# Kernel tuning notes

Measured on AMD Instinct MI355X. Metric: run time of the kernel, lower is better.

## Reference

```python
import jax, jax.numpy as jnp
import numpy as np

S, B, E, H = 2048, 2, 1024, 16
D = E // H  # head_dim


def setup_inputs() -> dict:
    key = jax.random.key(0)
    ks = jax.random.split(key, 12)
    scale = 1.0 / np.sqrt(E)
    inp = {
        "query": jax.random.normal(ks[0], (S, B, E), jnp.float32),
        "key_": jax.random.normal(ks[1], (S, B, E), jnp.float32),
        "value": jax.random.normal(ks[2], (S, B, E), jnp.float32),
        "Wq": jax.random.normal(ks[3], (E, E), jnp.float32) * scale,
        "bq": jax.random.normal(ks[4], (E,), jnp.float32) * scale,
        "Wk": jax.random.normal(ks[5], (E, E), jnp.float32) * scale,
        "bk": jax.random.normal(ks[6], (E,), jnp.float32) * scale,
        "Wv": jax.random.normal(ks[7], (E, E), jnp.float32) * scale,
        "bv": jax.random.normal(ks[8], (E,), jnp.float32) * scale,
        "Wo": jax.random.normal(ks[9], (E, E), jnp.float32) * scale,
        "bo": jax.random.normal(ks[10], (E,), jnp.float32) * scale,
        "bias_matrix": jax.random.normal(ks[11], (S, S), jnp.float32) * 0.1,
    }
    return inp


def _proj(x, W, b):
    # x: [S,B,E] -> linear -> [B,H,S,D]
    y = jnp.einsum('sbe,fe->sbf', x, W) + b  # torch Linear: x @ W.T + b
    return y.transpose(1, 0, 2).reshape(B, S, H, D).transpose(0, 2, 1, 3)


def reference(query, key_, value, Wq, bq, Wk, bk, Wv, bv, Wo, bo, bias_matrix):
    scaling = D ** -0.5
    Q = _proj(query, Wq, bq)   # [B,H,S,D]
    K = _proj(key_, Wk, bk)
    V = _proj(value, Wv, bv)
    scores = jnp.einsum('bhqd,bhkd->bhqk', Q, K) * scaling
    scores = scores + bias_matrix[None, None, :, :]
    attn = jax.nn.softmax(scores, axis=-1)  # dropout=0.0
    context = jnp.einsum('bhqk,bhkd->bhqd', attn, V)
    context = context.transpose(0, 2, 1, 3).reshape(B, S, E)
    out = jnp.einsum('bse,fe->bsf', context, Wo) + bo
    return out.transpose(1, 0, 2), attn  # ([S,B,E], [B,H,S,S])
```

## Files before the change

kernel.cpp:

```cpp
#include <hip/hip_runtime.h>

#define S_LEN 2048
#define B_SZ  2
#define E_SZ  1024
#define H_SZ  16
#define D_SZ  64

typedef __attribute__((ext_vector_type(8))) _Float16 f16x8;
typedef __attribute__((ext_vector_type(4))) _Float16 f16x4;
typedef __attribute__((ext_vector_type(4))) float    f32x4;

#define MFMA16(A,B,C) __builtin_amdgcn_mfma_f32_16x16x32_f16(A,B,C,0,0,0)

__device__ __forceinline__ void splitf(float x, _Float16& h, _Float16& l)
{
    _Float16 hh = (_Float16)x;
    h = hh;
    l = (_Float16)((x - (float)hh) * 2048.0f);
}

__device__ __forceinline__ void split_store4(float4 v, _Float16* ph, _Float16* pl)
{
    _Float16 h0,h1,h2,h3,l0,l1,l2,l3;
    splitf(v.x,h0,l0); splitf(v.y,h1,l1); splitf(v.z,h2,l2); splitf(v.w,h3,l3);
    *(f16x4*)ph = (f16x4){h0,h1,h2,h3};
    *(f16x4*)pl = (f16x4){l0,l1,l2,l3};
}

template<int VT>
__global__ __launch_bounds__(256, 2) void proj_qkv_mfma(
    const float* __restrict__ X,
    const float* __restrict__ W,
    const float* __restrict__ bias,
    _Float16* __restrict__ Oh, _Float16* __restrict__ Ol)
{
    __shared__ __align__(16) _Float16 sAh[64][32];
    __shared__ __align__(16) _Float16 sAl[64][32];
    __shared__ __align__(16) _Float16 sBh[128][32];
    __shared__ __align__(16) _Float16 sBl[128][32];

    const int t  = threadIdx.x;
    const int w  = t >> 6;
    const int l  = t & 63;
    const int lr = l & 15;
    const int lg = l >> 4;
    const int kb = lg * 8;
    const int m0 = blockIdx.y * 64;
    const int n0 = blockIdx.x * 128;

    const int srow = t >> 3;
    const int sc4  = (t & 7) * 4;

    f32x4 acc_h[4][2] = {};
    f32x4 acc_x[4][2] = {};

    for (int k0 = 0; k0 < E_SZ; k0 += 32) {
        #pragma unroll
        for (int i = 0; i < 2; ++i) {
            int row = srow + 32 * i;
            float4 v = *(const float4*)&X[(size_t)(m0 + row) * E_SZ + k0 + sc4];
            split_store4(v, &sAh[row][sc4], &sAl[row][sc4]);
        }
        #pragma unroll
        for (int i = 0; i < 4; ++i) {
            int row = srow + 32 * i;
            float4 v = *(const float4*)&W[(size_t)(n0 + row) * E_SZ + k0 + sc4];
            split_store4(v, &sBh[row][sc4], &sBl[row][sc4]);
        }
        __syncthreads();

        f16x8 fah[4], fal[4], fbh[2], fbl[2];
        #pragma unroll
        for (int mt = 0; mt < 4; ++mt) {
            fah[mt] = *(const f16x8*)&sAh[mt*16 + lr][kb];
            fal[mt] = *(const f16x8*)&sAl[mt*16 + lr][kb];
        }
        #pragma unroll
        for (int nt = 0; nt < 2; ++nt) {
            fbh[nt] = *(const f16x8*)&sBh[w*32 + nt*16 + lr][kb];
            fbl[nt] = *(const f16x8*)&sBl[w*32 + nt*16 + lr][kb];
        }
        #pragma unroll
        for (int mt = 0; mt < 4; ++mt)
            #pragma unroll
            for (int nt = 0; nt < 2; ++nt) {
                acc_h[mt][nt] = MFMA16(fah[mt], fbh[nt], acc_h[mt][nt]);
                acc_x[mt][nt] = MFMA16(fah[mt], fbl[nt], acc_x[mt][nt]);
                acc_x[mt][nt] = MFMA16(fal[mt], fbh[nt], acc_x[mt][nt]);
            }
        __syncthreads();
    }

    #pragma unroll
    for (int nt = 0; nt < 2; ++nt) {
        int c = n0 + w*32 + nt*16 + lr;
        float bv = bias[c];
        int hh = c >> 6, d = c & 63;
        #pragma unroll
        for (int mt = 0; mt < 4; ++mt)
            #pragma unroll
            for (int j = 0; j < 4; ++j) {
                int r = m0 + mt*16 + lg*4 + j;
                int s = r >> 1, b = r & 1;
                float v = acc_h[mt][nt][j] + acc_x[mt][nt][j] * (1.0f/2048.0f) + bv;
                _Float16 vh, vl; splitf(v, vh, vl);
                size_t idx = VT ? ((size_t)((b*H_SZ + hh)*D_SZ + d)) * S_LEN + s
                                : ((size_t)((b*H_SZ + hh)*S_LEN + s)) * D_SZ + d;
                Oh[idx] = vh; Ol[idx] = vl;
            }
    }
}

__global__ __launch_bounds__(256, 2) void proj_out_mfma(
    const float* __restrict__ X,
    const float* __restrict__ W,
    const float* __restrict__ bias,
    float* __restrict__ out)
{
    __shared__ __align__(16) _Float16 sAh[64][32];
    __shared__ __align__(16) _Float16 sAl[64][32];
    __shared__ __align__(16) _Float16 sBh[128][32];
    __shared__ __align__(16) _Float16 sBl[128][32];

    const int t  = threadIdx.x;
    const int w  = t >> 6;
    const int l  = t & 63;
    const int lr = l & 15;
    const int lg = l >> 4;
    const int kb = lg * 8;
    const int m0 = blockIdx.y * 64;
    const int n0 = blockIdx.x * 128;

    const int srow = t >> 3;
    const int sc4  = (t & 7) * 4;

    f32x4 acc_h[4][2] = {};
    f32x4 acc_x[4][2] = {};

    for (int k0 = 0; k0 < E_SZ; k0 += 32) {
        #pragma unroll
        for (int i = 0; i < 2; ++i) {
            int row = srow + 32 * i;
            float4 v = *(const float4*)&X[(size_t)(m0 + row) * E_SZ + k0 + sc4];
            split_store4(v, &sAh[row][sc4], &sAl[row][sc4]);
        }
        #pragma unroll
        for (int i = 0; i < 4; ++i) {
            int row = srow + 32 * i;
            float4 v = *(const float4*)&W[(size_t)(n0 + row) * E_SZ + k0 + sc4];
            split_store4(v, &sBh[row][sc4], &sBl[row][sc4]);
        }
        __syncthreads();

        f16x8 fah[4], fal[4], fbh[2], fbl[2];
        #pragma unroll
        for (int mt = 0; mt < 4; ++mt) {
            fah[mt] = *(const f16x8*)&sAh[mt*16 + lr][kb];
            fal[mt] = *(const f16x8*)&sAl[mt*16 + lr][kb];
        }
        #pragma unroll
        for (int nt = 0; nt < 2; ++nt) {
            fbh[nt] = *(const f16x8*)&sBh[w*32 + nt*16 + lr][kb];
            fbl[nt] = *(const f16x8*)&sBl[w*32 + nt*16 + lr][kb];
        }
        #pragma unroll
        for (int mt = 0; mt < 4; ++mt)
            #pragma unroll
            for (int nt = 0; nt < 2; ++nt) {
                acc_h[mt][nt] = MFMA16(fah[mt], fbh[nt], acc_h[mt][nt]);
                acc_x[mt][nt] = MFMA16(fah[mt], fbl[nt], acc_x[mt][nt]);
                acc_x[mt][nt] = MFMA16(fal[mt], fbh[nt], acc_x[mt][nt]);
            }
        __syncthreads();
    }

    #pragma unroll
    for (int nt = 0; nt < 2; ++nt) {
        int c = n0 + w*32 + nt*16 + lr;
        float bv = bias[c];
        #pragma unroll
        for (int mt = 0; mt < 4; ++mt)
            #pragma unroll
            for (int j = 0; j < 4; ++j) {
                int r = m0 + mt*16 + lg*4 + j;
                int b = r >> 11, s = r & 2047;
                float v = acc_h[mt][nt][j] + acc_x[mt][nt][j] * (1.0f/2048.0f) + bv;
                out[((size_t)s * B_SZ + b) * E_SZ + c] = v;
            }
    }
}

__global__ __launch_bounds__(256, 2) void scores_mfma(
    const _Float16* __restrict__ Qh, const _Float16* __restrict__ Ql,
    const _Float16* __restrict__ Kh, const _Float16* __restrict__ Kl,
    const float* __restrict__ biasM, float* __restrict__ attn)
{
    __shared__ __align__(16) _Float16 sQh[128][32];
    __shared__ __align__(16) _Float16 sQl[128][32];
    __shared__ __align__(16) _Float16 sKh[128][32];
    __shared__ __align__(16) _Float16 sKl[128][32];

    const int t  = threadIdx.x;
    const int w  = t >> 6;
    const int l  = t & 63;
    const int lr = l & 15;
    const int lg = l >> 4;
    const int kb = lg * 8;
    const int wm = w >> 1, wn = w & 1;
    const int kc0 = blockIdx.x * 128;
    const int q0  = blockIdx.y * 128;
    const int bh  = blockIdx.z;

    const _Float16* gQh = Qh + (size_t)(bh * S_LEN + q0)  * D_SZ;
    const _Float16* gQl = Ql + (size_t)(bh * S_LEN + q0)  * D_SZ;
    const _Float16* gKh = Kh + (size_t)(bh * S_LEN + kc0) * D_SZ;
    const _Float16* gKl = Kl + (size_t)(bh * S_LEN + kc0) * D_SZ;

    const int srow = t >> 2;
    const int sch  = (t & 3) * 8;

    f32x4 acc_h[4][4] = {};
    f32x4 acc_x[4][4] = {};

    #pragma unroll
    for (int k0 = 0; k0 < D_SZ; k0 += 32) {
        #pragma unroll
        for (int i = 0; i < 2; ++i) {
            int row = srow + 64 * i;
            *(f16x8*)&sQh[row][sch] = *(const f16x8*)&gQh[(size_t)row * D_SZ + k0 + sch];
            *(f16x8*)&sQl[row][sch] = *(const f16x8*)&gQl[(size_t)row * D_SZ + k0 + sch];
            *(f16x8*)&sKh[row][sch] = *(const f16x8*)&gKh[(size_t)row * D_SZ + k0 + sch];
            *(f16x8*)&sKl[row][sch] = *(const f16x8*)&gKl[(size_t)row * D_SZ + k0 + sch];
        }
        __syncthreads();

        f16x8 fah[4], fal[4], fbh[4], fbl[4];
        #pragma unroll
        for (int i = 0; i < 4; ++i) {
            fah[i] = *(const f16x8*)&sQh[wm*64 + i*16 + lr][kb];
            fal[i] = *(const f16x8*)&sQl[wm*64 + i*16 + lr][kb];
            fbh[i] = *(const f16x8*)&sKh[wn*64 + i*16 + lr][kb];
            fbl[i] = *(const f16x8*)&sKl[wn*64 + i*16 + lr][kb];
        }
        #pragma unroll
        for (int mt = 0; mt < 4; ++mt)
            #pragma unroll
            for (int nt = 0; nt < 4; ++nt) {
                acc_h[mt][nt] = MFMA16(fah[mt], fbh[nt], acc_h[mt][nt]);
                acc_x[mt][nt] = MFMA16(fah[mt], fbl[nt], acc_x[mt][nt]);
                acc_x[mt][nt] = MFMA16(fal[mt], fbh[nt], acc_x[mt][nt]);
            }
        __syncthreads();
    }

    const float scale = 0.125f;
    #pragma unroll
    for (int mt = 0; mt < 4; ++mt)
        #pragma unroll
        for (int j = 0; j < 4; ++j) {
            int q = q0 + wm*64 + mt*16 + lg*4 + j;
            const float* bR = biasM + (size_t)q * S_LEN;
            float* oR = attn + ((size_t)bh * S_LEN + q) * S_LEN;
            #pragma unroll
            for (int nt = 0; nt < 4; ++nt) {
                int kc = kc0 + wn*64 + nt*16 + lr;
                float v = acc_h[mt][nt][j] + acc_x[mt][nt][j] * (1.0f/2048.0f);
                oR[kc] = v * scale + bR[kc];
            }
        }
}

__global__ __launch_bounds__(256) void softmax_kernel(float* __restrict__ attn)
{
    const size_t row = blockIdx.x;
    float* p = attn + row * S_LEN;
    const int t = threadIdx.x;

    float4 v0 = *(const float4*)&p[t * 4];
    float4 v1 = *(const float4*)&p[1024 + t * 4];
    float v[8] = {v0.x, v0.y, v0.z, v0.w, v1.x, v1.y, v1.z, v1.w};

    float m = v[0];
    #pragma unroll
    for (int i = 1; i < 8; ++i) m = fmaxf(m, v[i]);
    #pragma unroll
    for (int off = 32; off; off >>= 1) m = fmaxf(m, __shfl_xor(m, off, 64));

    __shared__ float redm[4];
    __shared__ float reds[4];
    const int wave = t >> 6, lane = t & 63;
    if (lane == 0) redm[wave] = m;
    __syncthreads();
    m = fmaxf(fmaxf(redm[0], redm[1]), fmaxf(redm[2], redm[3]));

    float sum = 0.f;
    #pragma unroll
    for (int i = 0; i < 8; ++i) { v[i] = __expf(v[i] - m); sum += v[i]; }
    #pragma unroll
    for (int off = 32; off; off >>= 1) sum += __shfl_xor(sum, off, 64);
    if (lane == 0) reds[wave] = sum;
    __syncthreads();
    sum = reds[0] + reds[1] + reds[2] + reds[3];

    const float inv = 1.0f / sum;
    float4 o0 = make_float4(v[0]*inv, v[1]*inv, v[2]*inv, v[3]*inv);
    float4 o1 = make_float4(v[4]*inv, v[5]*inv, v[6]*inv, v[7]*inv);
    *(float4*)&p[t * 4]        = o0;
    *(float4*)&p[1024 + t * 4] = o1;
}

__global__ __launch_bounds__(256, 2) void context_mfma(
    const float* __restrict__ P,
    const _Float16* __restrict__ Vh,
    const _Float16* __restrict__ Vl,
    float* __restrict__ ctx)
{
    __shared__ __align__(16) _Float16 sPh[128][32];
    __shared__ __align__(16) _Float16 sPl[128][32];
    __shared__ __align__(16) _Float16 sVh[64][32];
    __shared__ __align__(16) _Float16 sVl[64][32];

    const int t  = threadIdx.x;
    const int w  = t >> 6;
    const int l  = t & 63;
    const int lr = l & 15;
    const int lg = l >> 4;
    const int kb = lg * 8;
    const int wm = w >> 1, wn = w & 1;
    const int q0 = blockIdx.x * 128;
    const int bh = blockIdx.y;
    const int b = bh >> 4, hd = bh & 15;

    const float* Pb = P + (size_t)(bh * S_LEN + q0) * S_LEN;
    const _Float16* gVh = Vh + (size_t)bh * D_SZ * S_LEN;
    const _Float16* gVl = Vl + (size_t)bh * D_SZ * S_LEN;

    const int prow = t >> 3, pc4 = (t & 7) * 4;
    const int vrow = t >> 2, vch = (t & 3) * 8;

    f32x4 acc_h[4][2] = {};
    f32x4 acc_x[4][2] = {};

    for (int k0 = 0; k0 < S_LEN; k0 += 32) {
        #pragma unroll
        for (int i = 0; i < 4; ++i) {
            int row = prow + 32 * i;
            float4 v = *(const float4*)&Pb[(size_t)row * S_LEN + k0 + pc4];
            split_store4(v, &sPh[row][pc4], &sPl[row][pc4]);
        }
        *(f16x8*)&sVh[vrow][vch] = *(const f16x8*)&gVh[(size_t)vrow * S_LEN + k0 + vch];
        *(f16x8*)&sVl[vrow][vch] = *(const f16x8*)&gVl[(size_t)vrow * S_LEN + k0 + vch];
        __syncthreads();

        f16x8 fah[4], fal[4], fbh[2], fbl[2];
        #pragma unroll
        for (int mt = 0; mt < 4; ++mt) {
            fah[mt] = *(const f16x8*)&sPh[wm*64 + mt*16 + lr][kb];
            fal[mt] = *(const f16x8*)&sPl[wm*64 + mt*16 + lr][kb];
        }
        #pragma unroll
        for (int nt = 0; nt < 2; ++nt) {
            fbh[nt] = *(const f16x8*)&sVh[wn*32 + nt*16 + lr][kb];
            fbl[nt] = *(const f16x8*)&sVl[wn*32 + nt*16 + lr][kb];
        }
        #pragma unroll
        for (int mt = 0; mt < 4; ++mt)
            #pragma unroll
            for (int nt = 0; nt < 2; ++nt) {
                acc_h[mt][nt] = MFMA16(fah[mt], fbh[nt], acc_h[mt][nt]);
                acc_x[mt][nt] = MFMA16(fah[mt], fbl[nt], acc_x[mt][nt]);
                acc_x[mt][nt] = MFMA16(fal[mt], fbh[nt], acc_x[mt][nt]);
            }
        __syncthreads();
    }

    #pragma unroll
    for (int mt = 0; mt < 4; ++mt)
        #pragma unroll
        for (int j = 0; j < 4; ++j) {
            int q = q0 + wm*64 + mt*16 + lg*4 + j;
            #pragma unroll
            for (int nt = 0; nt < 2; ++nt) {
                int d = wn*32 + nt*16 + lr;
                float v = acc_h[mt][nt][j] + acc_x[mt][nt][j] * (1.0f/2048.0f);
                ctx[((size_t)b * S_LEN + q) * E_SZ + hd * D_SZ + d] = v;
            }
        }
}

extern "C" void kernel_launch(void* const* d_in, const int* in_sizes, int n_in,
                              void* d_out, int out_size, void* d_ws, size_t ws_size,
                              hipStream_t stream)
{
    const float* query = (const float*)d_in[0];
    const float* key_  = (const float*)d_in[1];
    const float* value = (const float*)d_in[2];
    const float* Wq    = (const float*)d_in[3];
    const float* bq    = (const float*)d_in[4];
    const float* Wk    = (const float*)d_in[5];
    const float* bk    = (const float*)d_in[6];
    const float* Wv    = (const float*)d_in[7];
    const float* bv    = (const float*)d_in[8];
    const float* Wo    = (const float*)d_in[9];
    const float* bo    = (const float*)d_in[10];
    const float* biasM = (const float*)d_in[11];

    float* out  = (float*)d_out;
    float* attn = (float*)d_out + (size_t)S_LEN * B_SZ * E_SZ;

    const size_t qsz = (size_t)B_SZ * H_SZ * S_LEN * D_SZ;
    _Float16* ws16 = (_Float16*)d_ws;
    _Float16* Qh = ws16;
    _Float16* Ql = ws16 + qsz;
    _Float16* Kh = ws16 + 2 * qsz;
    _Float16* Kl = ws16 + 3 * qsz;
    _Float16* Vh = ws16 + 4 * qsz;
    _Float16* Vl = ws16 + 5 * qsz;
    float* ctx = (float*)(ws16 + 6 * qsz);

    dim3 gp(E_SZ / 128, (S_LEN * B_SZ) / 64);
    proj_qkv_mfma<0><<<gp, dim3(256), 0, stream>>>(query, Wq, bq, Qh, Ql);
    proj_qkv_mfma<0><<<gp, dim3(256), 0, stream>>>(key_,  Wk, bk, Kh, Kl);
    proj_qkv_mfma<1><<<gp, dim3(256), 0, stream>>>(value, Wv, bv, Vh, Vl);

    dim3 gsc(S_LEN / 128, S_LEN / 128, B_SZ * H_SZ);
    scores_mfma<<<gsc, dim3(256), 0, stream>>>(Qh, Ql, Kh, Kl, biasM, attn);

    softmax_kernel<<<dim3(B_SZ * H_SZ * S_LEN), dim3(256), 0, stream>>>(attn);

    dim3 gctx(S_LEN / 128, B_SZ * H_SZ);
    context_mfma<<<gctx, dim3(256), 0, stream>>>(attn, Vh, Vl, ctx);

    proj_out_mfma<<<gp, dim3(256), 0, stream>>>(ctx, Wo, bo, out);
}
```

Measured before the change: 1.461 ms.

## Pre-split inputs to fp16 pairs, enlarge GEMM tiles, pad LDS, drop P low part

```diff
diff --git a/kernel.cpp b/kernel.cpp
--- a/kernel.cpp
+++ b/kernel.cpp
@@ -11,6 +11,7 @@
 typedef __attribute__((ext_vector_type(4))) float    f32x4;
 
 #define MFMA16(A,B,C) __builtin_amdgcn_mfma_f32_16x16x32_f16(A,B,C,0,0,0)
+#define LPAD 40
 
 __device__ __forceinline__ void splitf(float x, _Float16& h, _Float16& l)
 {
@@ -27,63 +28,69 @@
     *(f16x4*)pl = (f16x4){l0,l1,l2,l3};
 }
 
+__global__ __launch_bounds__(256) void split_all(
+    const float* __restrict__ q, const float* __restrict__ k, const float* __restrict__ v,
+    const float* __restrict__ wq, const float* __restrict__ wk, const float* __restrict__ wv,
+    _Float16* __restrict__ H)
+{
+    const size_t M4 = 4194304, M1 = 1048576;
+    int blk = blockIdx.x;
+    const float* s; _Float16 *ph, *pl; size_t lb;
+    if      (blk < 2048) { s=q;  lb=blk;      ph=H;            pl=H+M4; }
+    else if (blk < 4096) { s=k;  lb=blk-2048; ph=H+2*M4;       pl=H+3*M4; }
+    else if (blk < 6144) { s=v;  lb=blk-4096; ph=H+4*M4;       pl=H+5*M4; }
+    else if (blk < 6656) { s=wq; lb=blk-6144; ph=H+6*M4;       pl=H+6*M4+M1; }
+    else if (blk < 7168) { s=wk; lb=blk-6656; ph=H+6*M4+2*M1;  pl=H+6*M4+3*M1; }
+    else                 { s=wv; lb=blk-7168; ph=H+6*M4+4*M1;  pl=H+6*M4+5*M1; }
+    size_t base = lb * 2048 + (size_t)threadIdx.x * 8;
+    float4 a = *(const float4*)&s[base];
+    float4 b = *(const float4*)&s[base + 4];
+    _Float16 h0,h1,h2,h3,h4,h5,h6,h7, l0,l1,l2,l3,l4,l5,l6,l7;
+    splitf(a.x,h0,l0); splitf(a.y,h1,l1); splitf(a.z,h2,l2); splitf(a.w,h3,l3);
+    splitf(b.x,h4,l4); splitf(b.y,h5,l5); splitf(b.z,h6,l6); splitf(b.w,h7,l7);
+    *(f16x8*)&ph[base] = (f16x8){h0,h1,h2,h3,h4,h5,h6,h7};
+    *(f16x8*)&pl[base] = (f16x8){l0,l1,l2,l3,l4,l5,l6,l7};
+}
+
 template<int VT>
-__global__ __launch_bounds__(256, 2) void proj_qkv_mfma(
-    const float* __restrict__ X,
-    const float* __restrict__ W,
+__global__ __launch_bounds__(256, 2) void proj_f16(
+    const _Float16* __restrict__ Ah, const _Float16* __restrict__ Al,
+    const _Float16* __restrict__ Bh, const _Float16* __restrict__ Bl,
     const float* __restrict__ bias,
     _Float16* __restrict__ Oh, _Float16* __restrict__ Ol)
 {
-    __shared__ __align__(16) _Float16 sAh[64][32];
-    __shared__ __align__(16) _Float16 sAl[64][32];
-    __shared__ __align__(16) _Float16 sBh[128][32];
-    __shared__ __align__(16) _Float16 sBl[128][32];
-
-    const int t  = threadIdx.x;
-    const int w  = t >> 6;
-    const int l  = t & 63;
-    const int lr = l & 15;
-    const int lg = l >> 4;
-    const int kb = lg * 8;
-    const int m0 = blockIdx.y * 64;
-    const int n0 = blockIdx.x * 128;
-
-    const int srow = t >> 3;
-    const int sc4  = (t & 7) * 4;
-
-    f32x4 acc_h[4][2] = {};
-    f32x4 acc_x[4][2] = {};
+    __shared__ __align__(16) _Float16 sAh[128][LPAD], sAl[128][LPAD];
+    __shared__ __align__(16) _Float16 sBh[128][LPAD], sBl[128][LPAD];
+    const int t = threadIdx.x, w = t >> 6, l = t & 63;
+    const int lr = l & 15, lg = l >> 4, kb = lg * 8;
+    const int wm = w >> 1, wn = w & 1;
+    const int m0 = blockIdx.y * 128, n0 = blockIdx.x * 128;
+    const int crow = t >> 2, ccol = (t & 3) * 8;
+
+    f32x4 acc_h[4][4] = {}, acc_x[4][4] = {};
 
     for (int k0 = 0; k0 < E_SZ; k0 += 32) {
         #pragma unroll
         for (int i = 0; i < 2; ++i) {
-            int row = srow + 32 * i;
-            float4 v = *(const float4*)&X[(size_t)(m0 + row) * E_SZ + k0 + sc4];
-            split_store4(v, &sAh[row][sc4], &sAl[row][sc4]);
-        }
+            int row = crow + 64 * i;
+            *(f16x8*)&sAh[row][ccol] = *(const f16x8*)&Ah[(size_t)(m0+row)*E_SZ + k0 + ccol];
+            *(f16x8*)&sAl[row][ccol] = *(const f16x8*)&Al[(size_t)(m0+row)*E_SZ + k0 + ccol];
+            *(f16x8*)&sBh[row][ccol] = *(const f16x8*)&Bh[(size_t)(n0+row)*E_SZ + k0 + ccol];
+            *(f16x8*)&sBl[row][ccol] = *(const f16x8*)&Bl[(size_t)(n0+row)*E_SZ + k0 + ccol];
+        }
+        __syncthreads();
+        f16x8 fah[4], fal[4], fbh[4], fbl[4];
         #pragma unroll
         for (int i = 0; i < 4; ++i) {
-            int row = srow + 32 * i;
-            float4 v = *(const float4*)&W[(size_t)(n0 + row) * E_SZ + k0 + sc4];
-            split_store4(v, &sBh[row][sc4], &sBl[row][sc4]);
-        }
-        __syncthreads();
-
-        f16x8 fah[4], fal[4], fbh[2], fbl[2];
-        #pragma unroll
-        for (int mt = 0; mt < 4; ++mt) {
-            fah[mt] = *(const f16x8*)&sAh[mt*16 + lr][kb];
-            fal[mt] = *(const f16x8*)&sAl[mt*16 + lr][kb];
-        }
-        #pragma unroll
-        for (int nt = 0; nt < 2; ++nt) {
-            fbh[nt] = *(const f16x8*)&sBh[w*32 + nt*16 + lr][kb];
-            fbl[nt] = *(const f16x8*)&sBl[w*32 + nt*16 + lr][kb];
-        }
-        #pragma unroll
-        for (int mt = 0; mt < 4; ++mt)
-            #pragma unroll
-            for (int nt = 0; nt < 2; ++nt) {
+            fah[i] = *(const f16x8*)&sAh[wm*64 + i*16 + lr][kb];
+            fal[i] = *(const f16x8*)&sAl[wm*64 + i*16 + lr][kb];
+            fbh[i] = *(const f16x8*)&sBh[wn*64 + i*16 + lr][kb];
+            fbl[i] = *(const f16x8*)&sBl[wn*64 + i*16 + lr][kb];
+        }
+        #pragma unroll
+        for (int mt = 0; mt < 4; ++mt)
+            #pragma unroll
+            for (int nt = 0; nt < 4; ++nt) {
                 acc_h[mt][nt] = MFMA16(fah[mt], fbh[nt], acc_h[mt][nt]);
                 acc_x[mt][nt] = MFMA16(fah[mt], fbl[nt], acc_x[mt][nt]);
                 acc_x[mt][nt] = MFMA16(fal[mt], fbh[nt], acc_x[mt][nt]);
@@ -92,18 +99,18 @@
     }
 
     #pragma unroll
-    for (int nt = 0; nt < 2; ++nt) {
-        int c = n0 + w*32 + nt*16 + lr;
+    for (int nt = 0; nt < 4; ++nt) {
+        int c = n0 + wn*64 + nt*16 + lr;
         float bv = bias[c];
         int hh = c >> 6, d = c & 63;
         #pragma unroll
         for (int mt = 0; mt < 4; ++mt)
             #pragma unroll
             for (int j = 0; j < 4; ++j) {
-                int r = m0 + mt*16 + lg*4 + j;
+                int r = m0 + wm*64 + mt*16 + lg*4 + j;
                 int s = r >> 1, b = r & 1;
-                float v = acc_h[mt][nt][j] + acc_x[mt][nt][j] * (1.0f/2048.0f) + bv;
-                _Float16 vh, vl; splitf(v, vh, vl);
+                float vv = acc_h[mt][nt][j] + acc_x[mt][nt][j] * (1.0f/2048.0f) + bv;
+                _Float16 vh, vl; splitf(vv, vh, vl);
                 size_t idx = VT ? ((size_t)((b*H_SZ + hh)*D_SZ + d)) * S_LEN + s
                                 : ((size_t)((b*H_SZ + hh)*S_LEN + s)) * D_SZ + d;
                 Oh[idx] = vh; Ol[idx] = vl;
@@ -111,62 +118,49 @@
     }
 }
 
-__global__ __launch_bounds__(256, 2) void proj_out_mfma(
-    const float* __restrict__ X,
+__global__ __launch_bounds__(256, 2) void proj_out_f16(
+    const _Float16* __restrict__ Ah, const _Float16* __restrict__ Al,
     const float* __restrict__ W,
     const float* __restrict__ bias,
     float* __restrict__ out)
 {
-    __shared__ __align__(16) _Float16 sAh[64][32];
-    __shared__ __align__(16) _Float16 sAl[64][32];
-    __shared__ __align__(16) _Float16 sBh[128][32];
-    __shared__ __align__(16) _Float16 sBl[128][32];
-
-    const int t  = threadIdx.x;
-    const int w  = t >> 6;
-    const int l  = t & 63;
-    const int lr = l & 15;
-    const int lg = l >> 4;
-    const int kb = lg * 8;
-    const int m0 = blockIdx.y * 64;
-    const int n0 = blockIdx.x * 128;
-
-    const int srow = t >> 3;
-    const int sc4  = (t & 7) * 4;
-
-    f32x4 acc_h[4][2] = {};
-    f32x4 acc_x[4][2] = {};
+    __shared__ __align__(16) _Float16 sAh[128][LPAD], sAl[128][LPAD];
+    __shared__ __align__(16) _Float16 sBh[128][LPAD], sBl[128][LPAD];
+    const int t = threadIdx.x, w = t >> 6, l = t & 63;
+    const int lr = l & 15, lg = l >> 4, kb = lg * 8;
+    const int wm = w >> 1, wn = w & 1;
+    const int m0 = blockIdx.y * 128, n0 = blockIdx.x * 128;
+    const int crow = t >> 2, ccol = (t & 3) * 8;
+    const int brow = t >> 3, bc4  = (t & 7) * 4;
+
+    f32x4 acc_h[4][4] = {}, acc_x[4][4] = {};
 
     for (int k0 = 0; k0 < E_SZ; k0 += 32) {
         #pragma unroll
         for (int i = 0; i < 2; ++i) {
-            int row = srow + 32 * i;
-            float4 v = *(const float4*)&X[(size_t)(m0 + row) * E_SZ + k0 + sc4];
-            split_store4(v, &sAh[row][sc4], &sAl[row][sc4]);
+            int row = crow + 64 * i;
+            *(f16x8*)&sAh[row][ccol] = *(const f16x8*)&Ah[(size_t)(m0+row)*E_SZ + k0 + ccol];
+            *(f16x8*)&sAl[row][ccol] = *(const f16x8*)&Al[(size_t)(m0+row)*E_SZ + k0 + ccol];
         }
         #pragma unroll
         for (int i = 0; i < 4; ++i) {
-            int row = srow + 32 * i;
-            float4 v = *(const float4*)&W[(size_t)(n0 + row) * E_SZ + k0 + sc4];
-            split_store4(v, &sBh[row][sc4], &sBl[row][sc4]);
-        }
-        __syncthreads();
-
-        f16x8 fah[4], fal[4], fbh[2], fbl[2];
-        #pragma unroll
-        for (int mt = 0; mt < 4; ++mt) {
-            fah[mt] = *(const f16x8*)&sAh[mt*16 + lr][kb];
-            fal[mt] = *(const f16x8*)&sAl[mt*16 + lr][kb];
-        }
-        #pragma unroll
-        for (int nt = 0; nt < 2; ++nt) {
-            fbh[nt] = *(const f16x8*)&sBh[w*32 + nt*16 + lr][kb];
-            fbl[nt] = *(const f16x8*)&sBl[w*32 + nt*16 + lr][kb];
-        }
-        #pragma unroll
-        for (int mt = 0; mt < 4; ++mt)
-            #pragma unroll
-            for (int nt = 0; nt < 2; ++nt) {
+            int row = brow + 32 * i;
+            float4 v = *(const float4*)&W[(size_t)(n0+row)*E_SZ + k0 + bc4];
+            split_store4(v, &sBh[row][bc4], &sBl[row][bc4]);
+        }
+        __syncthreads();
+        f16x8 fah[4], fal[4], fbh[4], fbl[4];
+        #pragma unroll
+        for (int i = 0; i < 4; ++i) {
+            fah[i] = *(const f16x8*)&sAh[wm*64 + i*16 + lr][kb];
+            fal[i] = *(const f16x8*)&sAl[wm*64 + i*16 + lr][kb];
+            fbh[i] = *(const f16x8*)&sBh[wn*64 + i*16 + lr][kb];
+            fbl[i] = *(const f16x8*)&sBl[wn*64 + i*16 + lr][kb];
+        }
+        #pragma unroll
+        for (int mt = 0; mt < 4; ++mt)
+            #pragma unroll
+            for (int nt = 0; nt < 4; ++nt) {
                 acc_h[mt][nt] = MFMA16(fah[mt], fbh[nt], acc_h[mt][nt]);
                 acc_x[mt][nt] = MFMA16(fah[mt], fbl[nt], acc_x[mt][nt]);
                 acc_x[mt][nt] = MFMA16(fal[mt], fbh[nt], acc_x[mt][nt]);
@@ -175,17 +169,17 @@
     }
 
     #pragma unroll
-    for (int nt = 0; nt < 2; ++nt) {
-        int c = n0 + w*32 + nt*16 + lr;
+    for (int nt = 0; nt < 4; ++nt) {
+        int c = n0 + wn*64 + nt*16 + lr;
         float bv = bias[c];
         #pragma unroll
         for (int mt = 0; mt < 4; ++mt)
             #pragma unroll
             for (int j = 0; j < 4; ++j) {
-                int r = m0 + mt*16 + lg*4 + j;
+                int r = m0 + wm*64 + mt*16 + lg*4 + j;
                 int b = r >> 11, s = r & 2047;
-                float v = acc_h[mt][nt][j] + acc_x[mt][nt][j] * (1.0f/2048.0f) + bv;
-                out[((size_t)s * B_SZ + b) * E_SZ + c] = v;
+                float vv = acc_h[mt][nt][j] + acc_x[mt][nt][j] * (1.0f/2048.0f) + bv;
+                out[((size_t)s * B_SZ + b) * E_SZ + c] = vv;
             }
     }
 }
@@ -195,32 +189,22 @@
     const _Float16* __restrict__ Kh, const _Float16* __restrict__ Kl,
     const float* __restrict__ biasM, float* __restrict__ attn)
 {
-    __shared__ __align__(16) _Float16 sQh[128][32];
-    __shared__ __align__(16) _Float16 sQl[128][32];
-    __shared__ __align__(16) _Float16 sKh[128][32];
-    __shared__ __align__(16) _Float16 sKl[128][32];
-
-    const int t  = threadIdx.x;
-    const int w  = t >> 6;
-    const int l  = t & 63;
-    const int lr = l & 15;
-    const int lg = l >> 4;
-    const int kb = lg * 8;
+    __shared__ __align__(16) _Float16 sQh[128][LPAD], sQl[128][LPAD];
+    __shared__ __align__(16) _Float16 sKh[128][LPAD], sKl[128][LPAD];
+    const int t = threadIdx.x, w = t >> 6, l = t & 63;
+    const int lr = l & 15, lg = l >> 4, kb = lg * 8;
     const int wm = w >> 1, wn = w & 1;
-    const int kc0 = blockIdx.x * 128;
-    const int q0  = blockIdx.y * 128;
-    const int bh  = blockIdx.z;
+    const int kc0 = blockIdx.x * 128, q0 = blockIdx.y * 128;
+    const int bh = blockIdx.z;
 
     const _Float16* gQh = Qh + (size_t)(bh * S_LEN + q0)  * D_SZ;
     const _Float16* gQl = Ql + (size_t)(bh * S_LEN + q0)  * D_SZ;
     const _Float16* gKh = Kh + (size_t)(bh * S_LEN + kc0) * D_SZ;
     const _Float16* gKl = Kl + (size_t)(bh * S_LEN + kc0) * D_SZ;
 
-    const int srow = t >> 2;
-    const int sch  = (t & 3) * 8;
-
-    f32x4 acc_h[4][4] = {};
-    f32x4 acc_x[4][4] = {};
+    const int srow = t >> 2, sch = (t & 3) * 8;
+
+    f32x4 acc_h[4][4] = {}, acc_x[4][4] = {};
 
     #pragma unroll
     for (int k0 = 0; k0 < D_SZ; k0 += 32) {
@@ -233,7 +217,6 @@
             *(f16x8*)&sKl[row][sch] = *(const f16x8*)&gKl[(size_t)row * D_SZ + k0 + sch];
         }
         __syncthreads();
-
         f16x8 fah[4], fal[4], fbh[4], fbl[4];
         #pragma unroll
         for (int i = 0; i < 4; ++i) {
@@ -311,21 +294,13 @@
 
 __global__ __launch_bounds__(256, 2) void context_mfma(
     const float* __restrict__ P,
-    const _Float16* __restrict__ Vh,
-    const _Float16* __restrict__ Vl,
-    float* __restrict__ ctx)
-{
-    __shared__ __align__(16) _Float16 sPh[128][32];
-    __shared__ __align__(16) _Float16 sPl[128][32];
-    __shared__ __align__(16) _Float16 sVh[64][32];
-    __shared__ __align__(16) _Float16 sVl[64][32];
-
-    const int t  = threadIdx.x;
-    const int w  = t >> 6;
-    const int l  = t & 63;
-    const int lr = l & 15;
-    const int lg = l >> 4;
-    const int kb = lg * 8;
+    const _Float16* __restrict__ Vh, const _Float16* __restrict__ Vl,
+    _Float16* __restrict__ Ch, _Float16* __restrict__ Cl)
+{
+    __shared__ __align__(16) _Float16 sPh[128][LPAD];
+    __shared__ __align__(16) _Float16 sVh[64][LPAD], sVl[64][LPAD];
+    const int t = threadIdx.x, w = t >> 6, l = t & 63;
+    const int lr = l & 15, lg = l >> 4, kb = lg * 8;
     const int wm = w >> 1, wn = w & 1;
     const int q0 = blockIdx.x * 128;
     const int bh = blockIdx.y;
@@ -338,38 +313,35 @@
     const int prow = t >> 3, pc4 = (t & 7) * 4;
     const int vrow = t >> 2, vch = (t & 3) * 8;
 
-    f32x4 acc_h[4][2] = {};
-    f32x4 acc_x[4][2] = {};
+    f32x4 acc_h[4][2] = {}, acc_x[4][2] = {};
 
     for (int k0 = 0; k0 < S_LEN; k0 += 32) {
         #pragma unroll
         for (int i = 0; i < 4; ++i) {
             int row = prow + 32 * i;
             float4 v = *(const float4*)&Pb[(size_t)row * S_LEN + k0 + pc4];
-            split_store4(v, &sPh[row][pc4], &sPl[row][pc4]);
+            _Float16 p0 = (_Float16)v.x, p1 = (_Float16)v.y,
+                     p2 = (_Float16)v.z, p3 = (_Float16)v.w;
+            *(f16x4*)&sPh[row][pc4] = (f16x4){p0,p1,p2,p3};
         }
         *(f16x8*)&sVh[vrow][vch] = *(const f16x8*)&gVh[(size_t)vrow * S_LEN + k0 + vch];
         *(f16x8*)&sVl[vrow][vch] = *(const f16x8*)&gVl[(size_t)vrow * S_LEN + k0 + vch];
         __syncthreads();
-
-        f16x8 fah[4], fal[4], fbh[2], fbl[2];
-        #pragma unroll
-        for (int mt = 0; mt < 4; ++mt) {
-            fah[mt] = *(const f16x8*)&sPh[wm*64 + mt*16 + lr][kb];
-            fal[mt] = *(const f16x8*)&sPl[wm*64 + mt*16 + lr][kb];
-        }
+        f16x8 pa[4], vbh[2], vbl[2];
+        #pragma unroll
+        for (int mt = 0; mt < 4; ++mt)
+            pa[mt] = *(const f16x8*)&sPh[wm*64 + mt*16 + lr][kb];
         #pragma unroll
         for (int nt = 0; nt < 2; ++nt) {
-            fbh[nt] = *(const f16x8*)&sVh[wn*32 + nt*16 + lr][kb];
-            fbl[nt] = *(const f16x8*)&sVl[wn*32 + nt*16 + lr][kb];
+            vbh[nt] = *(const f16x8*)&sVh[wn*32 + nt*16 + lr][kb];
+            vbl[nt] = *(const f16x8*)&sVl[wn*32 + nt*16 + lr][kb];
         }
         #pragma unroll
         for (int mt = 0; mt < 4; ++mt)
             #pragma unroll
             for (int nt = 0; nt < 2; ++nt) {
-                acc_h[mt][nt] = MFMA16(fah[mt], fbh[nt], acc_h[mt][nt]);
-                acc_x[mt][nt] = MFMA16(fah[mt], fbl[nt], acc_x[mt][nt]);
-                acc_x[mt][nt] = MFMA16(fal[mt], fbh[nt], acc_x[mt][nt]);
+                acc_h[mt][nt] = MFMA16(pa[mt], vbh[nt], acc_h[mt][nt]);
+                acc_x[mt][nt] = MFMA16(pa[mt], vbl[nt], acc_x[mt][nt]);
             }
         __syncthreads();
     }
@@ -382,8 +354,10 @@
             #pragma unroll
             for (int nt = 0; nt < 2; ++nt) {
                 int d = wn*32 + nt*16 + lr;
-                float v = acc_h[mt][nt][j] + acc_x[mt][nt][j] * (1.0f/2048.0f);
-                ctx[((size_t)b * S_LEN + q) * E_SZ + hd * D_SZ + d] = v;
+                float vv = acc_h[mt][nt][j] + acc_x[mt][nt][j] * (1.0f/2048.0f);
+                _Float16 vh, vl; splitf(vv, vh, vl);
+                size_t idx = ((size_t)b * S_LEN + q) * E_SZ + hd * D_SZ + d;
+                Ch[idx] = vh; Cl[idx] = vl;
             }
         }
 }
@@ -408,20 +382,28 @@
     float* out  = (float*)d_out;
     float* attn = (float*)d_out + (size_t)S_LEN * B_SZ * E_SZ;
 
+    _Float16* scratch = (_Float16*)attn;
+    const size_t M4 = 4194304, M1 = 1048576;
+    _Float16* Xq_h = scratch;            _Float16* Xq_l = scratch + M4;
+    _Float16* Xk_h = scratch + 2*M4;     _Float16* Xk_l = scratch + 3*M4;
+    _Float16* Xv_h = scratch + 4*M4;     _Float16* Xv_l = scratch + 5*M4;
+    _Float16* Wq_h = scratch + 6*M4;          _Float16* Wq_l = Wq_h + M1;
+    _Float16* Wk_h = scratch + 6*M4 + 2*M1;   _Float16* Wk_l = Wk_h + M1;
+    _Float16* Wv_h = scratch + 6*M4 + 4*M1;   _Float16* Wv_l = Wv_h + M1;
+
     const size_t qsz = (size_t)B_SZ * H_SZ * S_LEN * D_SZ;
     _Float16* ws16 = (_Float16*)d_ws;
-    _Float16* Qh = ws16;
-    _Float16* Ql = ws16 + qsz;
-    _Float16* Kh = ws16 + 2 * qsz;
-    _Float16* Kl = ws16 + 3 * qsz;
-    _Float16* Vh = ws16 + 4 * qsz;
-    _Float16* Vl = ws16 + 5 * qsz;
-    float* ctx = (float*)(ws16 + 6 * qsz);
-
-    dim3 gp(E_SZ / 128, (S_LEN * B_SZ) / 64);
-    proj_qkv_mfma<0><<<gp, dim3(256), 0, stream>>>(query, Wq, bq, Qh, Ql);
-    proj_qkv_mfma<0><<<gp, dim3(256), 0, stream>>>(key_,  Wk, bk, Kh, Kl);
-    proj_qkv_mfma<1><<<gp, dim3(256), 0, stream>>>(value, Wv, bv, Vh, Vl);
+    _Float16* Qh = ws16;            _Float16* Ql = ws16 + qsz;
+    _Float16* Kh = ws16 + 2*qsz;    _Float16* Kl = ws16 + 3*qsz;
+    _Float16* Vh = ws16 + 4*qsz;    _Float16* Vl = ws16 + 5*qsz;
+    _Float16* Ch = ws16 + 6*qsz;    _Float16* Cl = ws16 + 7*qsz;
+
+    split_all<<<dim3(7680), dim3(256), 0, stream>>>(query, key_, value, Wq, Wk, Wv, scratch);
+
+    dim3 gp(E_SZ / 128, (S_LEN * B_SZ) / 128);
+    proj_f16<0><<<gp, dim3(256), 0, stream>>>(Xq_h, Xq_l, Wq_h, Wq_l, bq, Qh, Ql);
+    proj_f16<0><<<gp, dim3(256), 0, stream>>>(Xk_h, Xk_l, Wk_h, Wk_l, bk, Kh, Kl);
+    proj_f16<1><<<gp, dim3(256), 0, stream>>>(Xv_h, Xv_l, Wv_h, Wv_l, bv, Vh, Vl);
 
     dim3 gsc(S_LEN / 128, S_LEN / 128, B_SZ * H_SZ);
     scores_mfma<<<gsc, dim3(256), 0, stream>>>(Qh, Ql, Kh, Kl, biasM, attn);
@@ -429,7 +411,7 @@
     softmax_kernel<<<dim3(B_SZ * H_SZ * S_LEN), dim3(256), 0, stream>>>(attn);
 
     dim3 gctx(S_LEN / 128, B_SZ * H_SZ);
-    context_mfma<<<gctx, dim3(256), 0, stream>>>(attn, Vh, Vl, ctx);
-
-    proj_out_mfma<<<gp, dim3(256), 0, stream>>>(ctx, Wo, bo, out);
-}
+    context_mfma<<<gctx, dim3(256), 0, stream>>>(attn, Vh, Vl, Ch, Cl);
+
+    proj_out_f16<<<gp, dim3(256), 0, stream>>>(Ch, Cl, Wo, bo, out);
+}
```

Result: faster. 1.253 ms (-14.2%).
